# Kernel tuning notes

Hardware: AMD Instinct MI355X
Metric: run time of the kernel (lower is better)

The kernel has to match this reference:

```python
import jax, jax.numpy as jnp
import numpy as np
from jax import lax

# Dims: B=batch, Cin=in_channel, Ch=channel (bottleneck), Br=breadth (num expert kernels)
B, Cin, Ch, Br, H, W = 16, 256, 128, 8, 64, 64


def setup_inputs() -> dict:
    key = jax.random.key(0)
    ks = jax.random.split(key, 6)
    sc = lambda k, shape: jax.random.normal(k, shape, jnp.float32) * 0.05
    return {
        "x": jax.random.normal(ks[0], (B, Cin, H, W), jnp.float32),
        # SwitchedConv #1: 3x3, in_channel -> channel, breadth expert kernels
        "W1": sc(ks[1], (Br, Ch, Cin, 3, 3)),
        "b1": jnp.zeros((Ch,), jnp.float32),
        # lambda coupler #1: 1x1 projection in_channel -> breadth (per-pixel routing)
        "Wc1": sc(ks[2], (Br, Cin)),
        "bc1": jnp.zeros((Br,), jnp.float32),
        # SwitchedConv #2: 1x1, channel -> in_channel
        "W2": sc(ks[3], (Br, Cin, Ch, 1, 1)),
        "b2": jnp.zeros((Cin,), jnp.float32),
        # lambda coupler #2: 1x1 projection channel -> breadth
        "Wc2": sc(ks[4], (Br, Ch)),
        "bc2": jnp.zeros((Br,), jnp.float32),
    }


def _switched_conv(x, Wk, b, Wc, bc, pad):
    """Input-conditioned mixture of `breadth` conv kernels.

    The coupler (1x1 projection of x to breadth logits, softmax over breadth)
    produces per-pixel mixture weights; each expert kernel's conv output is
    combined per-pixel with these weights.
    x: [B, Cin, H, W]; Wk: [Br, Cout, Cin, k, k]
    """
    br, cout, cin, k, _ = Wk.shape
    bsz, _, h, w = x.shape
    # per-pixel routing weights over the breadth dim: [B, Br, H, W]
    sel = jax.nn.softmax(jnp.einsum('bihw,gi->bghw', x, Wc) + bc[None, :, None, None], axis=1)
    # all breadth branches in one grouped-output conv: [B, Br*Cout, H, W]
    y = lax.conv_general_dilated(
        x, Wk.reshape(br * cout, cin, k, k),
        window_strides=(1, 1), padding=[(pad, pad), (pad, pad)],
        dimension_numbers=('NCHW', 'OIHW', 'NCHW'))
    y = y.reshape(bsz, br, cout, h, w)
    # selection-weighted reduction over breadth + bias
    return jnp.einsum('bgchw,bghw->bchw', y, sel) + b[None, :, None, None]


def reference(x, W1, b1, Wc1, bc1, W2, b2, Wc2, bc2):
    h = jax.nn.relu(x)
    h = _switched_conv(h, W1, b1, Wc1, bc1, pad=1)  # 3x3 switched conv
    h = jax.nn.relu(h)
    h = _switched_conv(h, W2, b2, Wc2, bc2, pad=0)  # 1x1 switched conv
    return h + x  # residual add
```

## Files before the change

### kernel.cpp

```cpp
#include <hip/hip_runtime.h>
#include <hip/hip_bf16.h>
#include <cstdint>

typedef _Float16 h8 __attribute__((ext_vector_type(8)));
typedef _Float16 h4 __attribute__((ext_vector_type(4)));
typedef float    f4 __attribute__((ext_vector_type(4)));
typedef float    fx16 __attribute__((ext_vector_type(16)));


#define GLD16(src, dst) __builtin_amdgcn_global_load_lds( \
    (const __attribute__((address_space(1))) void*)(src), \
    (__attribute__((address_space(3))) void*)(dst), 16, 0, 0)

__global__ __launch_bounds__(256) void prep_w_k(const float* __restrict__ W1,
        const float* __restrict__ W2, _Float16* __restrict__ W1r,
        _Float16* __restrict__ W2r) {
    int o8 = blockIdx.x * 256 + threadIdx.x;
    if (o8 < 294912) {
        int sq = o8 & 3;
        int c  = (o8 >> 2) & 127;
        int g  = (o8 >> 9) & 7;
        int tk = o8 >> 12;
        int tap = tk % 9, cik = tk / 9;
        int s = sq ^ ((c >> 1) & 3);
        int ci0 = cik * 32 + s * 8;
        const float* src = W1 + ((size_t)(g * 128 + c) * 256 + ci0) * 9 + tap;
        h8 v;
        #pragma unroll
        for (int e = 0; e < 8; ++e) v[e] = (_Float16)src[e * 9];
        *(h8*)(W1r + (size_t)o8 * 8) = v;
    } else {
        int ow = o8 - 294912;
        int sg = ow & 3;
        int co = (ow >> 2) & 255;
        int kc = (ow >> 10) & 3;
        int g  = ow >> 12;
        const float* src = W2 + ((size_t)(g * 256 + co) * 128) + kc * 32 + sg * 8;
        h8 v;
        #pragma unroll
        for (int e = 0; e < 8; ++e) v[e] = (_Float16)src[e];
        *(h8*)(W2r + (size_t)ow * 8) = v;
    }
}

__global__ __launch_bounds__(256) void prep_x_k(const float* __restrict__ x,
        const float* __restrict__ Wc1, const float* __restrict__ bc1,
        float* __restrict__ sel1) {
    __shared__ float wc[2048];
    int t = threadIdx.x;
    for (int i = t; i < 2048; i += 256) wc[i] = Wc1[i];
    __syncthreads();
    int pix = blockIdx.x * 256 + t;
    int b = pix >> 12, p = pix & 4095;
    const float* xp = x + (size_t)b * 1048576 + p;
    float lg[8] = {0.f,0.f,0.f,0.f,0.f,0.f,0.f,0.f};
    for (int c = 0; c < 256; ++c) {
        float v = fmaxf(xp[(size_t)c * 4096], 0.f);
        #pragma unroll
        for (int g = 0; g < 8; ++g) lg[g] += wc[g * 256 + c] * v;
    }
    float m = -1e30f;
    #pragma unroll
    for (int g = 0; g < 8; ++g) { lg[g] += bc1[g]; m = fmaxf(m, lg[g]); }
    float sum = 0.f;
    #pragma unroll
    for (int g = 0; g < 8; ++g) { lg[g] = __expf(lg[g] - m); sum += lg[g]; }
    float inv = 1.f / sum;
    #pragma unroll
    for (int g = 0; g < 8; ++g)
        sel1[(size_t)(b * 8 + g) * 4096 + p] = lg[g] * inv;
}

__global__ __launch_bounds__(512, 2) void conv1_k(const float* __restrict__ x,
        const _Float16* __restrict__ W1r, const float* __restrict__ sel1,
        const float* __restrict__ b1, _Float16* __restrict__ hr) {
    __shared__ _Float16 wt[3][16384];
    __shared__ _Float16 xs[12296];
    int t = threadIdx.x;
    int b = blockIdx.y, yt = blockIdx.x;
    int y0 = yt * 4;
    int w = t >> 6, l = t & 63;
    int wm = w >> 2, wn = w & 3;
    int l31 = l & 31, kq2 = l >> 5;
    if (t < 8) xs[12288 + t] = (_Float16)0.f;

    fx16 acc[2][2];
    #pragma unroll
    for (int m = 0; m < 2; ++m)
        #pragma unroll
        for (int n = 0; n < 2; ++n)
            #pragma unroll
            for (int e = 0; e < 16; ++e) acc[m][n][e] = 0.f;

    auto stage_w = [&](int P, int bi) {
        const _Float16* srcw = W1r + (size_t)P * 16384 + t * 8;
        _Float16* dw = wt[bi] + t * 8;
        #pragma unroll
        for (int it = 0; it < 4; ++it)
            GLD16(srcw + it * 4096, dw + it * 4096);
    };

    int px[2];
    #pragma unroll
    for (int nf = 0; nf < 2; ++nf) px[nf] = wn * 64 + nf * 32 + l31;
    bool e0 = (l31 == 0), e63 = (l31 == 31);
    int afo[2][2];
    #pragma unroll
    for (int m = 0; m < 2; ++m)
        #pragma unroll
        for (int kc = 0; kc < 2; ++kc) {
            int c = wm * 64 + m * 32 + l31;
            afo[m][kc] = c * 32 + (((kc * 2 + kq2) ^ ((c >> 1) & 3)) * 8);
        }
    int ba[2][3][2];
    #pragma unroll
    for (int nf = 0; nf < 2; ++nf)
        #pragma unroll
        for (int kx = 0; kx < 3; ++kx) {
            int rz = px[nf] + kx - 1;
            #pragma unroll
            for (int kc = 0; kc < 2; ++kc)
                ba[nf][kx][kc] = rz * 32 + (((kc * 2 + kq2) ^ ((rz >> 1) & 3)) * 8);
        }
    h8 selv[2];
    #pragma unroll
    for (int nf = 0; nf < 2; ++nf)
        #pragma unroll
        for (int g = 0; g < 8; ++g)
            selv[nf][g] = (_Float16)sel1[(size_t)(b * 8 + g) * 4096 + yt * 256 + px[nf]];

    h8 bfr[2][2];

    stage_w(0, 0);
    stage_w(1, 1);

    #pragma unroll 1
    for (int ci = 0; ci < 8; ++ci) {
        if (t < 384) {
            int r = t >> 6, col = t & 63;
            int rc = r * 64 + col;
            int yi = y0 - 1 + r;
            _Float16* dx = xs + rc * 32;
            int rx = (rc >> 1) & 3;
            if (yi >= 0 && yi < 64) {
                const float* xp = x + ((size_t)(b * 256 + ci * 32)) * 4096 + yi * 64 + col;
                float v[32];
                #pragma unroll
                for (int c2 = 0; c2 < 32; ++c2)
                    v[c2] = fmaxf(xp[(size_t)c2 * 4096], 0.f);
                #pragma unroll
                for (int qq = 0; qq < 4; ++qq) {
                    h8 hv;
                    #pragma unroll
                    for (int e = 0; e < 8; ++e) hv[e] = (_Float16)v[qq * 8 + e];
                    *(h8*)(dx + (qq ^ rx) * 8) = hv;
                }
            } else {
                const h8 HZ = {};
                #pragma unroll
                for (int qq = 0; qq < 4; ++qq)
                    *(h8*)(dx + (qq ^ rx) * 8) = HZ;
            }
        }
        __syncthreads();
        #pragma unroll 1
        for (int ky = 0; ky < 3; ++ky) {
            #pragma unroll
            for (int kx = 0; kx < 3; ++kx) {
                int tap = ci * 9 + ky * 3 + kx;
                #pragma unroll
                for (int nf = 0; nf < 2; ++nf)
                    #pragma unroll
                    for (int kc = 0; kc < 2; ++kc) {
                        int a = ba[nf][kx][kc] + ky * 2048;
                        if (kx == 0 && nf == 0) a = e0 ? 12288 : a;
                        if (kx == 2 && nf == 1) a = e63 ? 12288 : a;
                        bfr[nf][kc] = *(const h8*)(xs + a);
                    }
                #pragma unroll
                for (int gp = 0; gp < 2; ++gp) {
                    int P = tap * 2 + gp;
                    __builtin_amdgcn_s_barrier();
                    if (P >= 143) {
                        asm volatile("s_waitcnt vmcnt(0)" ::: "memory");
                    } else {
                        asm volatile("s_waitcnt vmcnt(4)" ::: "memory");
                    }
                    __builtin_amdgcn_sched_barrier(0);
                    const _Float16* wp = wt[(2 * kx + gp) % 3];
                    __builtin_amdgcn_s_setprio(1);
                    #pragma unroll
                    for (int gl = 0; gl < 4; ++gl) {
                        #pragma unroll
                        for (int kc = 0; kc < 2; ++kc) {
                            h8 a0 = *(const h8*)(wp + gl * 4096 + afo[0][kc]);
                            h8 a1 = *(const h8*)(wp + gl * 4096 + afo[1][kc]);
                            #pragma unroll
                            for (int nf = 0; nf < 2; ++nf) {
                                h8 bs = bfr[nf][kc] * selv[nf][gp * 4 + gl];
                                acc[0][nf] = __builtin_amdgcn_mfma_f32_32x32x16_f16(
                                    a0, bs, acc[0][nf], 0, 0, 0);
                                acc[1][nf] = __builtin_amdgcn_mfma_f32_32x32x16_f16(
                                    a1, bs, acc[1][nf], 0, 0, 0);
                            }
                        }
                    }
                    __builtin_amdgcn_s_setprio(0);
                    if (P < 142) stage_w(P + 2, (2 * kx + gp + 2) % 3);
                }
            }
        }
    }
    #pragma unroll
    for (int m = 0; m < 2; ++m)
        #pragma unroll
        for (int nf = 0; nf < 2; ++nf) {
            size_t pg = ((size_t)(b * 4096 + yt * 256 + px[nf])) * 128;
            #pragma unroll
            for (int q = 0; q < 4; ++q) {
                int c0 = wm * 64 + m * 32 + q * 8 + kq2 * 4;
                f4 bb = *(const f4*)(b1 + c0);
                h4 hv;
                #pragma unroll
                for (int r = 0; r < 4; ++r)
                    hv[r] = (_Float16)fmaxf(acc[m][nf][q * 4 + r] + bb[r], 0.f);
                *(h4*)(hr + pg + c0) = hv;
            }
        }
}

__global__ __launch_bounds__(256, 2) void conv2_k(const _Float16* __restrict__ hr,
        const _Float16* __restrict__ W2r, const float* __restrict__ Wc2,
        const float* __restrict__ bc2, const float* __restrict__ b2,
        const float* __restrict__ x, float* __restrict__ out) {
    __shared__ _Float16 hs[64 * 128];
    __shared__ _Float16 wt[2][256 * 32];
    __shared__ float wc[1024];
    __shared__ float red[2048];
    __shared__ float selw[512];
    int t = threadIdx.x;
    int bid = blockIdx.x;
    int b = bid >> 6, p0 = (bid & 63) * 64;
    int l = t & 63, w = t >> 6;
    int wm = w >> 1, wn = w & 1;
    int l15 = l & 15, sl = l >> 4;
    int swl = (l15 & 7) << 3;
    const f4 FZ = {0.f, 0.f, 0.f, 0.f};
    f4 acce[8][2], accf[8][2];
    #pragma unroll
    for (int m = 0; m < 8; ++m)
        #pragma unroll
        for (int n = 0; n < 2; ++n) { acce[m][n] = FZ; accf[m][n] = FZ; }
    for (int i = t; i < 1024; i += 256) wc[i] = Wc2[i];
    {
        int px = t >> 2, qq = t & 3;
        const _Float16* src = hr + (size_t)(b * 4096 + p0 + px) * 128 + qq * 32;
        #pragma unroll
        for (int u = 0; u < 4; ++u)
            *(h8*)(hs + ((px * 128 + qq * 32 + u * 8) ^ ((px & 7) << 3)))
                = *(const h8*)(src + u * 8);
    }
    h8 wr[4];
    auto load_w = [&](int T) {
        const _Float16* srcw = W2r + (size_t)T * 8192;
        #pragma unroll
        for (int it = 0; it < 4; ++it)
            wr[it] = *(const h8*)(srcw + (size_t)(it * 256 + t) * 8);
    };
    auto write_w = [&](int bf) {
        #pragma unroll
        for (int it = 0; it < 4; ++it) {
            int cc = it * 256 + t;
            int c = cc >> 2, q = cc & 3;
            *(h8*)(wt[bf] + ((c * 32 + q * 8) ^ ((c & 7) << 3))) = wr[it];
        }
    };
    load_w(0);
    __syncthreads();
    {
        int px = t >> 2, qq = t & 3;
        float lg[8] = {0.f,0.f,0.f,0.f,0.f,0.f,0.f,0.f};
        #pragma unroll
        for (int u = 0; u < 4; ++u) {
            h8 v = *(const h8*)(hs + ((px * 128 + qq * 32 + u * 8) ^ ((px & 7) << 3)));
            #pragma unroll
            for (int e = 0; e < 8; ++e) {
                float f = (float)v[e];
                int c = qq * 32 + u * 8 + e;
                #pragma unroll
                for (int g = 0; g < 8; ++g) lg[g] += wc[g * 128 + c] * f;
            }
        }
        #pragma unroll
        for (int g = 0; g < 8; ++g) red[(px * 8 + g) * 4 + qq] = lg[g];
    }
    __syncthreads();
    if (t < 64) {
        float lg[8]; float m = -1e30f;
        #pragma unroll
        for (int g = 0; g < 8; ++g) {
            lg[g] = red[(t*8+g)*4+0] + red[(t*8+g)*4+1]
                  + red[(t*8+g)*4+2] + red[(t*8+g)*4+3] + bc2[g];
            m = fmaxf(m, lg[g]);
        }
        float sum = 0.f;
        #pragma unroll
        for (int g = 0; g < 8; ++g) { lg[g] = __expf(lg[g] - m); sum += lg[g]; }
        float inv = 1.f / sum;
        #pragma unroll
        for (int g = 0; g < 8; ++g) selw[t * 8 + g] = lg[g] * inv;
    }
    write_w(0);
    __syncthreads();
    float selr[8][2];
    #pragma unroll
    for (int g = 0; g < 8; ++g)
        #pragma unroll
        for (int n = 0; n < 2; ++n)
            selr[g][n] = selw[(wn * 32 + n * 16 + l15) * 8 + g];
    int afo[8];
    #pragma unroll
    for (int m = 0; m < 8; ++m) {
        int c = wm * 128 + m * 16 + l15;
        afo[m] = ((c * 32 + sl * 8) ^ swl);
    }
    int buf = 0;
    #pragma unroll 1
    for (int T = 0; T < 32; ++T) {
        bool hn = (T < 31);
        if (hn) load_w(T + 1);
        __syncthreads();
        int kc = (T & 3) * 32;
        h8 bfv[2];
        #pragma unroll
        for (int n = 0; n < 2; ++n) {
            int px = wn * 32 + n * 16 + l15;
            bfv[n] = *(const h8*)(hs + ((px * 128 + kc + sl * 8) ^ ((px & 7) << 3)));
        }
        #pragma unroll
        for (int m = 0; m < 8; ++m) {
            h8 af = *(const h8*)(wt[buf] + afo[m]);
            #pragma unroll
            for (int n = 0; n < 2; ++n)
                acce[m][n] = __builtin_amdgcn_mfma_f32_16x16x32_f16(
                    af, bfv[n], acce[m][n], 0, 0, 0);
        }
        if ((T & 3) == 3) {
            int g = T >> 2;
            #pragma unroll
            for (int n = 0; n < 2; ++n)
                #pragma unroll
                for (int m = 0; m < 8; ++m) {
                    accf[m][n] += selr[g][n] * acce[m][n];
                    acce[m][n] = FZ;
                }
        }
        if (hn) write_w(buf ^ 1);
        buf ^= 1;
    }
    #pragma unroll
    for (int m = 0; m < 8; ++m) {
        int c0 = wm * 128 + m * 16 + sl * 4;
        f4 bb = *(const f4*)(b2 + c0);
        #pragma unroll
        for (int n = 0; n < 2; ++n) {
            int px = wn * 32 + n * 16 + l15;
            size_t o = (size_t)(b * 256 + c0) * 4096 + p0 + px;
            #pragma unroll
            for (int r = 0; r < 4; ++r)
                out[o + (size_t)r * 4096] = accf[m][n][r] + bb[r] + x[o + (size_t)r * 4096];
        }
    }
}

extern "C" void kernel_launch(void* const* d_in, const int* in_sizes, int n_in,
                              void* d_out, int out_size, void* d_ws, size_t ws_size,
                              hipStream_t stream) {
    const float* x   = (const float*)d_in[0];
    const float* W1  = (const float*)d_in[1];
    const float* b1  = (const float*)d_in[2];
    const float* Wc1 = (const float*)d_in[3];
    const float* bc1 = (const float*)d_in[4];
    const float* W2  = (const float*)d_in[5];
    const float* b2  = (const float*)d_in[6];
    const float* Wc2 = (const float*)d_in[7];
    const float* bc2 = (const float*)d_in[8];
    float* out = (float*)d_out;
    char* ws = (char*)d_ws;
    _Float16* hr  = (_Float16*)(ws);
    _Float16* W1r = (_Float16*)(ws + 16777216);
    _Float16* W2r = (_Float16*)(ws + 21495808);
    float* sel1   = (float*)(ws + 22020096);

    hipLaunchKernelGGL(prep_w_k, dim3(1280), dim3(256), 0, stream, W1, W2, W1r, W2r);
    hipLaunchKernelGGL(prep_x_k, dim3(256), dim3(256), 0, stream, x, Wc1, bc1, sel1);
    hipLaunchKernelGGL(conv1_k, dim3(16, 16), dim3(512), 0, stream, x, W1r, sel1, b1, hr);
    hipLaunchKernelGGL(conv2_k, dim3(1024), dim3(256), 0, stream, hr, W2r, Wc2, bc2, b2, x, out);
}
```

Baseline: 345.2 us.

## Pipeline conv2 weights via direct global-to-LDS loads and split prep_x channels

conv2 now streams expert weight tiles straight into LDS with global_load_lds into a triple buffer, with the bank swizzle moved into the host-side prep of W2. This replaces the register round trip, and the loop uses explicit vmcnt waits, one barrier and raised priority around the MFMAs. prep_x splits the channel reduction across two thread halves with an LDS reduction, doubling the grid to expose more parallelism in the memory-bound logits pass. This costs extra LDS for a third weight buffer and relies on hand-counted waitcnt values.

```diff
diff --git a/kernel.cpp b/kernel.cpp
--- a/kernel.cpp
+++ b/kernel.cpp
@@ -31,11 +31,12 @@
         *(h8*)(W1r + (size_t)o8 * 8) = v;
     } else {
         int ow = o8 - 294912;
-        int sg = ow & 3;
+        int sq = ow & 3;
         int co = (ow >> 2) & 255;
         int kc = (ow >> 10) & 3;
         int g  = ow >> 12;
-        const float* src = W2 + ((size_t)(g * 256 + co) * 128) + kc * 32 + sg * 8;
+        int s = sq ^ ((co >> 1) & 3);
+        const float* src = W2 + ((size_t)(g * 256 + co) * 128) + kc * 32 + s * 8;
         h8 v;
         #pragma unroll
         for (int e = 0; e < 8; ++e) v[e] = (_Float16)src[e];
@@ -47,28 +48,39 @@
         const float* __restrict__ Wc1, const float* __restrict__ bc1,
         float* __restrict__ sel1) {
     __shared__ float wc[2048];
+    __shared__ float red[1024];
     int t = threadIdx.x;
     for (int i = t; i < 2048; i += 256) wc[i] = Wc1[i];
     __syncthreads();
-    int pix = blockIdx.x * 256 + t;
+    int pxl = t & 127, ch = t >> 7;
+    int pix = blockIdx.x * 128 + pxl;
     int b = pix >> 12, p = pix & 4095;
-    const float* xp = x + (size_t)b * 1048576 + p;
+    const float* xp = x + (size_t)b * 1048576 + (size_t)ch * 524288 + p;
     float lg[8] = {0.f,0.f,0.f,0.f,0.f,0.f,0.f,0.f};
-    for (int c = 0; c < 256; ++c) {
+    for (int c = 0; c < 128; ++c) {
         float v = fmaxf(xp[(size_t)c * 4096], 0.f);
         #pragma unroll
-        for (int g = 0; g < 8; ++g) lg[g] += wc[g * 256 + c] * v;
-    }
-    float m = -1e30f;
-    #pragma unroll
-    for (int g = 0; g < 8; ++g) { lg[g] += bc1[g]; m = fmaxf(m, lg[g]); }
-    float sum = 0.f;
-    #pragma unroll
-    for (int g = 0; g < 8; ++g) { lg[g] = __expf(lg[g] - m); sum += lg[g]; }
-    float inv = 1.f / sum;
-    #pragma unroll
-    for (int g = 0; g < 8; ++g)
-        sel1[(size_t)(b * 8 + g) * 4096 + p] = lg[g] * inv;
+        for (int g = 0; g < 8; ++g) lg[g] += wc[g * 256 + ch * 128 + c] * v;
+    }
+    if (ch)
+        #pragma unroll
+        for (int g = 0; g < 8; ++g) red[pxl * 8 + g] = lg[g];
+    __syncthreads();
+    if (!ch) {
+        float m = -1e30f;
+        #pragma unroll
+        for (int g = 0; g < 8; ++g) {
+            lg[g] += red[pxl * 8 + g] + bc1[g];
+            m = fmaxf(m, lg[g]);
+        }
+        float sum = 0.f;
+        #pragma unroll
+        for (int g = 0; g < 8; ++g) { lg[g] = __expf(lg[g] - m); sum += lg[g]; }
+        float inv = 1.f / sum;
+        #pragma unroll
+        for (int g = 0; g < 8; ++g)
+            sel1[(size_t)(b * 8 + g) * 4096 + p] = lg[g] * inv;
+    }
 }
 
 __global__ __launch_bounds__(512, 2) void conv1_k(const float* __restrict__ x,
@@ -234,7 +246,7 @@
         const float* __restrict__ bc2, const float* __restrict__ b2,
         const float* __restrict__ x, float* __restrict__ out) {
     __shared__ _Float16 hs[64 * 128];
-    __shared__ _Float16 wt[2][256 * 32];
+    __shared__ _Float16 wt[3][8192];
     __shared__ float wc[1024];
     __shared__ float red[2048];
     __shared__ float selw[512];
@@ -244,13 +256,23 @@
     int l = t & 63, w = t >> 6;
     int wm = w >> 1, wn = w & 1;
     int l15 = l & 15, sl = l >> 4;
-    int swl = (l15 & 7) << 3;
     const f4 FZ = {0.f, 0.f, 0.f, 0.f};
     f4 acce[8][2], accf[8][2];
     #pragma unroll
     for (int m = 0; m < 8; ++m)
         #pragma unroll
         for (int n = 0; n < 2; ++n) { acce[m][n] = FZ; accf[m][n] = FZ; }
+
+    auto stage_w = [&](int T, int bi) {
+        const _Float16* srcw = W2r + (size_t)T * 8192 + t * 8;
+        _Float16* dw = wt[bi] + t * 8;
+        #pragma unroll
+        for (int it = 0; it < 4; ++it)
+            GLD16(srcw + it * 2048, dw + it * 2048);
+    };
+    stage_w(0, 0);
+    stage_w(1, 1);
+
     for (int i = t; i < 1024; i += 256) wc[i] = Wc2[i];
     {
         int px = t >> 2, qq = t & 3;
@@ -260,22 +282,6 @@
             *(h8*)(hs + ((px * 128 + qq * 32 + u * 8) ^ ((px & 7) << 3)))
                 = *(const h8*)(src + u * 8);
     }
-    h8 wr[4];
-    auto load_w = [&](int T) {
-        const _Float16* srcw = W2r + (size_t)T * 8192;
-        #pragma unroll
-        for (int it = 0; it < 4; ++it)
-            wr[it] = *(const h8*)(srcw + (size_t)(it * 256 + t) * 8);
-    };
-    auto write_w = [&](int bf) {
-        #pragma unroll
-        for (int it = 0; it < 4; ++it) {
-            int cc = it * 256 + t;
-            int c = cc >> 2, q = cc & 3;
-            *(h8*)(wt[bf] + ((c * 32 + q * 8) ^ ((c & 7) << 3))) = wr[it];
-        }
-    };
-    load_w(0);
     __syncthreads();
     {
         int px = t >> 2, qq = t & 3;
@@ -310,7 +316,6 @@
         #pragma unroll
         for (int g = 0; g < 8; ++g) selw[t * 8 + g] = lg[g] * inv;
     }
-    write_w(0);
     __syncthreads();
     float selr[8][2];
     #pragma unroll
@@ -322,14 +327,18 @@
     #pragma unroll
     for (int m = 0; m < 8; ++m) {
         int c = wm * 128 + m * 16 + l15;
-        afo[m] = ((c * 32 + sl * 8) ^ swl);
-    }
-    int buf = 0;
+        afo[m] = c * 32 + ((sl ^ ((c >> 1) & 3)) * 8);
+    }
     #pragma unroll 1
     for (int T = 0; T < 32; ++T) {
-        bool hn = (T < 31);
-        if (hn) load_w(T + 1);
-        __syncthreads();
+        __builtin_amdgcn_s_barrier();
+        if (T >= 31) {
+            asm volatile("s_waitcnt vmcnt(0)" ::: "memory");
+        } else {
+            asm volatile("s_waitcnt vmcnt(4)" ::: "memory");
+        }
+        __builtin_amdgcn_sched_barrier(0);
+        const _Float16* wp = wt[0] + (size_t)(T % 3) * 8192;
         int kc = (T & 3) * 32;
         h8 bfv[2];
         #pragma unroll
@@ -337,14 +346,16 @@
             int px = wn * 32 + n * 16 + l15;
             bfv[n] = *(const h8*)(hs + ((px * 128 + kc + sl * 8) ^ ((px & 7) << 3)));
         }
+        __builtin_amdgcn_s_setprio(1);
         #pragma unroll
         for (int m = 0; m < 8; ++m) {
-            h8 af = *(const h8*)(wt[buf] + afo[m]);
+            h8 af = *(const h8*)(wp + afo[m]);
             #pragma unroll
             for (int n = 0; n < 2; ++n)
                 acce[m][n] = __builtin_amdgcn_mfma_f32_16x16x32_f16(
                     af, bfv[n], acce[m][n], 0, 0, 0);
         }
+        __builtin_amdgcn_s_setprio(0);
         if ((T & 3) == 3) {
             int g = T >> 2;
             #pragma unroll
@@ -355,8 +366,7 @@
                     acce[m][n] = FZ;
                 }
         }
-        if (hn) write_w(buf ^ 1);
-        buf ^= 1;
+        if (T < 30) stage_w(T + 2, (T + 2) % 3);
     }
     #pragma unroll
     for (int m = 0; m < 8; ++m) {
@@ -393,7 +403,7 @@
     float* sel1   = (float*)(ws + 22020096);
 
     hipLaunchKernelGGL(prep_w_k, dim3(1280), dim3(256), 0, stream, W1, W2, W1r, W2r);
-    hipLaunchKernelGGL(prep_x_k, dim3(256), dim3(256), 0, stream, x, Wc1, bc1, sel1);
+    hipLaunchKernelGGL(prep_x_k, dim3(512), dim3(256), 0, stream, x, Wc1, bc1, sel1);
     hipLaunchKernelGGL(conv1_k, dim3(16, 16), dim3(512), 0, stream, x, W1r, sel1, b1, hr);
     hipLaunchKernelGGL(conv2_k, dim3(1024), dim3(256), 0, stream, hr, W2r, Wc2, bc2, b2, x, out);
 }
```

New measurement: 334.9 us. 3.0% less time.
